# Kernel tuning notes

Measured on AMD Instinct MI355X. Metric: run time of the kernel, lower is better.

## Reference

```python
import jax, jax.numpy as jnp
import numpy as np

B, S, HIDDEN = 2, 2048, 2048
NUM_HEADS, NUM_KV_HEADS, HEAD_DIM = 16, 4, 128
Q_SIZE = NUM_HEADS * HEAD_DIM          # 2048
KV_SIZE = NUM_KV_HEADS * HEAD_DIM      # 512
ROPE_THETA = 10000.0
NEG = -1e30


def setup_inputs() -> dict:
    key = jax.random.key(0)
    k1, k2, k3 = jax.random.split(key, 3)
    hidden_states = jax.random.normal(k1, (B, S, HIDDEN), jnp.float32)
    w_qkv = jax.random.normal(k2, (HIDDEN, Q_SIZE + 2 * KV_SIZE), jnp.float32) / np.sqrt(HIDDEN)
    w_o = jax.random.normal(k3, (Q_SIZE, HIDDEN), jnp.float32) / np.sqrt(Q_SIZE)
    positions = jnp.broadcast_to(jnp.arange(S, dtype=jnp.int32), (B, S))
    return {"positions": positions, "hidden_states": hidden_states,
            "w_qkv": w_qkv, "w_o": w_o}


def _rope(x, positions):
    # x: [B, S, H, D], neox-style rotate-half rope over full head_dim
    d = x.shape[-1]
    inv_freq = 1.0 / (ROPE_THETA ** (jnp.arange(0, d, 2, dtype=jnp.float32) / d))
    ang = positions[..., None].astype(jnp.float32) * inv_freq      # [B, S, D/2]
    cos = jnp.cos(ang)[:, :, None, :]
    sin = jnp.sin(ang)[:, :, None, :]
    x1, x2 = jnp.split(x, 2, axis=-1)
    return jnp.concatenate([x1 * cos - x2 * sin, x2 * cos + x1 * sin], axis=-1)


def reference(positions, hidden_states, w_qkv, w_o):
    qkv = jnp.einsum('bsh,ho->bso', hidden_states, w_qkv)
    q, k, v = jnp.split(qkv, [Q_SIZE, Q_SIZE + KV_SIZE], axis=-1)
    q = q.reshape(B, S, NUM_HEADS, HEAD_DIM)
    k = k.reshape(B, S, NUM_KV_HEADS, HEAD_DIM)
    v = v.reshape(B, S, NUM_KV_HEADS, HEAD_DIM)
    q = _rope(q, positions)
    k = _rope(k, positions)
    rep = NUM_HEADS // NUM_KV_HEADS
    k = jnp.repeat(k, rep, axis=2)   # GQA expand -> [B, S, NUM_HEADS, D]
    v = jnp.repeat(v, rep, axis=2)
    scale = HEAD_DIM ** -0.5
    scores = jnp.einsum('bqhd,bkhd->bhqk', q, k) * scale   # [B, H, S, S]
    causal = jnp.tril(jnp.ones((S, S), dtype=bool))
    scores = jnp.where(causal, scores, NEG)
    probs = jax.nn.softmax(scores, axis=-1)
    attn = jnp.einsum('bhqk,bkhd->bqhd', probs, v).reshape(B, S, Q_SIZE)
    return jnp.einsum('bsq,qh->bsh', attn, w_o)
```

## Files before the change

### kernel.cpp

```cpp
#include <hip/hip_runtime.h>
#include <hip/hip_bf16.h>
#include <stdint.h>

#define BDIM 2
#define SDIM 2048
#define HID 2048
#define NH 16
#define NKV 4
#define HD 128
#define QSZ 2048
#define KVSZ 512
#define QKVW 3072
#define TOK (BDIM*SDIM)

typedef __attribute__((ext_vector_type(8))) short bf16x8;
typedef __attribute__((ext_vector_type(4))) float f32x4;
typedef __attribute__((ext_vector_type(16))) float f32x16;

__device__ __forceinline__ short f2bf(float f) {
  return (short)__bfloat16_as_ushort(__float2bfloat16(f));
}

__device__ __forceinline__ float exp2_fast(float x) {
  float r;
  asm("v_exp_f32 %0, %1" : "=v"(r) : "v"(x));
  return r;
}

__device__ __forceinline__ void sincos_rev(float rev, float* sn, float* cs) {
  float fr, s, c;
  asm("v_fract_f32 %0, %1" : "=v"(fr) : "v"(rev));
  asm("v_sin_f32 %0, %1" : "=v"(s) : "v"(fr));
  asm("v_cos_f32 %0, %1" : "=v"(c) : "v"(fr));
  *sn = s; *cs = c;
}

__device__ __forceinline__ int xcd_swz(int orig, int nwg) {
  int cpx = nwg >> 3;
  return (orig & 7) * cpx + (orig >> 3);
}

__device__ __forceinline__ void gload_lds16(const void* g, void* lds) {
  __builtin_amdgcn_global_load_lds(
      (const __attribute__((address_space(1))) void*)g,
      (__attribute__((address_space(3))) void*)lds, 16, 0, 0);
}

__global__ __launch_bounds__(256) void k_cvt_bf16(const float* __restrict__ in,
                                                  short* __restrict__ out, int n) {
  int i = (blockIdx.x * 256 + threadIdx.x) * 4;
  if (i >= n) return;
  float4 v = *(const float4*)(in + i);
  short4 o; o.x = f2bf(v.x); o.y = f2bf(v.y); o.z = f2bf(v.z); o.w = f2bf(v.w);
  *(short4*)(out + i) = o;
}

__global__ __launch_bounds__(256) void k_transpose_cvt(const float* __restrict__ in,
                                                       short* __restrict__ out,
                                                       int R, int C) {
  __shared__ short tile[64][65];
  int k0 = blockIdx.y * 64;
  int n0 = blockIdx.x * 64;
  int t = threadIdx.x;
#pragma unroll
  for (int i = 0; i < 16; ++i) {
    int idx = i * 256 + t;
    int kk = idx >> 6, nn = idx & 63;
    tile[kk][nn] = f2bf(in[(size_t)(k0 + kk) * C + n0 + nn]);
  }
  __syncthreads();
#pragma unroll
  for (int i = 0; i < 16; ++i) {
    int idx = i * 256 + t;
    int nn = idx >> 6, kk = idx & 63;
    out[(size_t)(n0 + nn) * R + k0 + kk] = tile[kk][nn];
  }
}

__global__ __launch_bounds__(256) void k_gemm_bf16(const short* __restrict__ A,
                                                   const short* __restrict__ Bt,
                                                   float* __restrict__ C,
                                                   int M, int N, int K) {
  __shared__ char lds[128 * 32 * 2 * 2];
  char* As = lds;
  char* Bs = lds + 8192;
  const int tid = threadIdx.x;
  const int w = tid >> 6, l = tid & 63;
  const int lq = l & 15, g = l >> 4;
  const int nx = N >> 7;
  const int bid = xcd_swz(blockIdx.x, nx * (M >> 7));
  const int m0 = (bid / nx) * 128, n0 = (bid % nx) * 128;
  const int wm = (w >> 1) * 64, wn = (w & 1) * 64;
  f32x4 acc[4][4] = {};

  const int nk = K >> 5;
  for (int kt = 0; kt < nk; ++kt) {
    const int k0 = kt * 32;
#pragma unroll
    for (int i = 0; i < 2; ++i) {
      int ch = (w + 4 * i) * 64 + l;
      int r = ch >> 2, cc = ch & 3;
      int gc = cc ^ ((r >> 1) & 3);
      gload_lds16(A + (size_t)(m0 + r) * K + k0 + gc * 8, As + (w + 4 * i) * 1024);
      gload_lds16(Bt + (size_t)(n0 + r) * K + k0 + gc * 8, Bs + (w + 4 * i) * 1024);
    }
    __syncthreads();
    bf16x8 af[4], bfr[4];
#pragma unroll
    for (int mi = 0; mi < 4; ++mi) {
      int row = wm + mi * 16 + lq;
      af[mi] = *(const bf16x8*)(As + row * 64 + ((g ^ ((row >> 1) & 3)) * 16));
    }
#pragma unroll
    for (int ni = 0; ni < 4; ++ni) {
      int row = wn + ni * 16 + lq;
      bfr[ni] = *(const bf16x8*)(Bs + row * 64 + ((g ^ ((row >> 1) & 3)) * 16));
    }
#pragma unroll
    for (int mi = 0; mi < 4; ++mi)
#pragma unroll
      for (int ni = 0; ni < 4; ++ni)
        acc[mi][ni] = __builtin_amdgcn_mfma_f32_16x16x32_bf16(af[mi], bfr[ni],
                                                              acc[mi][ni], 0, 0, 0);
    __syncthreads();
  }
#pragma unroll
  for (int mi = 0; mi < 4; ++mi)
#pragma unroll
    for (int ni = 0; ni < 4; ++ni)
#pragma unroll
      for (int r = 0; r < 4; ++r) {
        int row = m0 + wm + mi * 16 + 4 * g + r;
        int col = n0 + wn + ni * 16 + lq;
        C[(size_t)row * N + col] = acc[mi][ni][r];
      }
}

__global__ __launch_bounds__(256) void k_gemm_qkv_rope(const short* __restrict__ A,
                                                       const short* __restrict__ Bt,
                                                       const int* __restrict__ pos,
                                                       short* __restrict__ Qh,
                                                       short* __restrict__ Kh,
                                                       short* __restrict__ VT) {
  __shared__ char lds[128 * 32 * 2 * 2];
  char* As = lds;
  char* Bs = lds + 8192;
  const int tid = threadIdx.x;
  const int w = tid >> 6, l = tid & 63;
  const int lq = l & 15, g = l >> 4;
  const int bid = xcd_swz(blockIdx.x, (QKVW >> 7) * (TOK >> 7));
  const int hx = bid % (QKVW >> 7);
  const int m0 = (bid / (QKVW >> 7)) * 128, n0 = hx * 128;
  const int K = HID;
  f32x4 acc[2][8] = {};

  const int nk = K >> 5;
  for (int kt = 0; kt < nk; ++kt) {
    const int k0 = kt * 32;
#pragma unroll
    for (int i = 0; i < 2; ++i) {
      int ch = (w + 4 * i) * 64 + l;
      int r = ch >> 2, cc = ch & 3;
      int gc = cc ^ ((r >> 1) & 3);
      gload_lds16(A + (size_t)(m0 + r) * K + k0 + gc * 8, As + (w + 4 * i) * 1024);
      gload_lds16(Bt + (size_t)(n0 + r) * K + k0 + gc * 8, Bs + (w + 4 * i) * 1024);
    }
    __syncthreads();
    bf16x8 af[2], bfr[8];
#pragma unroll
    for (int mi = 0; mi < 2; ++mi) {
      int row = w * 32 + mi * 16 + lq;
      af[mi] = *(const bf16x8*)(As + row * 64 + ((g ^ ((row >> 1) & 3)) * 16));
    }
#pragma unroll
    for (int ni = 0; ni < 8; ++ni) {
      int row = ni * 16 + lq;
      bfr[ni] = *(const bf16x8*)(Bs + row * 64 + ((g ^ ((row >> 1) & 3)) * 16));
    }
#pragma unroll
    for (int mi = 0; mi < 2; ++mi)
#pragma unroll
      for (int ni = 0; ni < 8; ++ni)
        acc[mi][ni] = __builtin_amdgcn_mfma_f32_16x16x32_bf16(af[mi], bfr[ni],
                                                              acc[mi][ni], 0, 0, 0);
    __syncthreads();
  }

  const int b = m0 >> 11;
  if (hx < 20) {
    const float qscale = 0.12751743920f;
    const float sc = (hx < 16) ? qscale : 1.0f;
    short* dst = (hx < 16) ? (Qh + (size_t)(b * NH + hx) * SDIM * HD)
                           : (Kh + (size_t)(b * NKV + (hx - 16)) * SDIM * HD);
    float invf[4];
#pragma unroll
    for (int ni = 0; ni < 4; ++ni)
      invf[ni] = 0.15915494309f *
                 exp2_fast(-(float)(ni * 16 + lq) * (13.287712379549449f / 64.0f));
#pragma unroll
    for (int mi = 0; mi < 2; ++mi)
#pragma unroll
      for (int r = 0; r < 4; ++r) {
        int row = m0 + w * 32 + mi * 16 + 4 * g + r;
        int s = row & (SDIM - 1);
        float p = (float)pos[row];
        size_t hb = (size_t)s * HD;
#pragma unroll
        for (int ni = 0; ni < 4; ++ni) {
          float sn, cs;
          sincos_rev(p * invf[ni], &sn, &cs);
          float x1 = acc[mi][ni][r], x2 = acc[mi][ni + 4][r];
          dst[hb + ni * 16 + lq] = f2bf((x1 * cs - x2 * sn) * sc);
          dst[hb + ni * 16 + lq + 64] = f2bf((x2 * cs + x1 * sn) * sc);
        }
      }
  } else {
    const int hv = hx - 20;
    const int s00 = (m0 & (SDIM - 1)) + w * 32;
#pragma unroll
    for (int mi = 0; mi < 2; ++mi)
#pragma unroll
      for (int ni = 0; ni < 8; ++ni) {
        int d = ni * 16 + lq;
        int s0 = s00 + mi * 16 + 4 * g;
        size_t vb = ((size_t)(b * NKV + hv) * HD + d) * SDIM + s0;
        short4 ov;
        ov.x = f2bf(acc[mi][ni][0]); ov.y = f2bf(acc[mi][ni][1]);
        ov.z = f2bf(acc[mi][ni][2]); ov.w = f2bf(acc[mi][ni][3]);
        *(short4*)(VT + vb) = ov;
      }
  }
}

__global__ __launch_bounds__(256, 2) void k_attn(const short* __restrict__ Qh,
                                                 const short* __restrict__ Kh,
                                                 const short* __restrict__ VT,
                                                 short* __restrict__ attn, int S) {
  __shared__ char lds[2][32768];
  const int tid = threadIdx.x;
  const int w = tid >> 6, l = tid & 63;
  const int l31 = l & 31, hi = l >> 5;
  const int nqc = S / 128;
  const int bid = blockIdx.x;
  const int b = bid / (NH * nqc);
  const int rem = bid % (NH * nqc);
  const int h = rem / nqc;
  const int qc = nqc - 1 - (rem % nqc);
  const int q0 = qc * 128 + w * 32;
  const int kvh = h >> 2;
  const short* Qp = Qh + (size_t)(b * NH + h) * S * HD;
  const short* Kp = Kh + (size_t)(b * NKV + kvh) * S * HD;
  const short* Vp = VT + (size_t)(b * NKV + kvh) * HD * S;

  bf16x8 qf[8];
#pragma unroll
  for (int kc = 0; kc < 8; ++kc)
    qf[kc] = *(const bf16x8*)(Qp + (size_t)(q0 + l31) * HD + kc * 16 + hi * 8);

  f32x16 o[4] = {};
  float mrun = -1e30f, lrun = 0.f;
  const int qabs = q0 + l31;
  const int ntu = qc * 2 + 2;

#define STAGE(bufi, c0_)                                                          \
  {                                                                               \
    char* Kb = lds[bufi];                                                         \
    char* Vb = lds[bufi] + 16384;                                                 \
    _Pragma("unroll")                                                             \
    for (int i = 0; i < 4; ++i) {                                                 \
      int id = (i * 4 + w) * 64 + l;                                              \
      int kr = id >> 4, c16 = id & 15;                                            \
      gload_lds16(Kp + (size_t)((c0_) + kr) * HD + ((c16 ^ (kr & 15)) * 8),       \
                  Kb + (i * 4 + w) * 1024);                                       \
      int vr = id >> 3, c8 = id & 7;                                              \
      gload_lds16(Vp + (size_t)vr * S + (c0_) + ((c8 ^ (vr & 7)) * 8),            \
                  Vb + (i * 4 + w) * 1024);                                       \
    }                                                                             \
  }

  STAGE(0, 0);
  asm volatile("s_waitcnt vmcnt(0)" ::: "memory");
  __builtin_amdgcn_s_barrier();

  for (int c = 0; c < ntu; ++c) {
    const int c0 = c * 64;
    const int cur = c & 1;
    if (c + 1 < ntu) STAGE(cur ^ 1, c0 + 64);
    const char* Ks = lds[cur];
    const char* Vs = lds[cur] + 16384;

    f32x16 st[2];
    __builtin_amdgcn_s_setprio(1);
#pragma unroll
    for (int tt = 0; tt < 2; ++tt) {
      f32x16 s = {};
#pragma unroll
      for (int kc = 0; kc < 8; ++kc) {
        int kr = tt * 32 + l31;
        bf16x8 kf = *(const bf16x8*)(Ks + kr * 256 + (((kc * 2 + hi) ^ (l31 & 15)) * 16));
        s = __builtin_amdgcn_mfma_f32_32x32x16_bf16(kf, qf[kc], s, 0, 0, 0);
      }
      st[tt] = s;
    }
    __builtin_amdgcn_s_setprio(0);
    float tmax = -1e30f;
    if (c0 + 64 <= q0) {
#pragma unroll
      for (int tt = 0; tt < 2; ++tt)
#pragma unroll
        for (int r = 0; r < 16; ++r) tmax = fmaxf(tmax, st[tt][r]);
    } else {
#pragma unroll
      for (int tt = 0; tt < 2; ++tt)
#pragma unroll
        for (int r = 0; r < 16; ++r) {
          int kv = c0 + tt * 32 + (r & 3) + 8 * (r >> 2) + 4 * hi;
          float sv = (kv <= qabs) ? st[tt][r] : -1e30f;
          st[tt][r] = sv;
          tmax = fmaxf(tmax, sv);
        }
    }
    tmax = fmaxf(tmax, __shfl_xor(tmax, 32));
    if (!__all(tmax - mrun <= 8.0f)) {
      float mnew = fmaxf(mrun, tmax);
      float fac = exp2_fast(mrun - mnew);
      lrun *= fac;
#pragma unroll
      for (int d0 = 0; d0 < 4; ++d0) o[d0] = o[d0] * fac;
      mrun = mnew;
    }
    float sum = 0.f;
#pragma unroll
    for (int tt = 0; tt < 2; ++tt)
#pragma unroll
      for (int r = 0; r < 16; ++r) {
        float e = exp2_fast(st[tt][r] - mrun);
        st[tt][r] = e;
        sum += e;
      }
    sum += __shfl_xor(sum, 32);
    lrun += sum;
    __builtin_amdgcn_s_setprio(1);
#pragma unroll
    for (int j = 0; j < 4; ++j) {
      const int tt = j >> 1, kc = j & 1;
      uint32_t W0 = (uint32_t)(uint16_t)f2bf(st[tt][8 * kc + 0]) |
                    ((uint32_t)(uint16_t)f2bf(st[tt][8 * kc + 1]) << 16);
      uint32_t W1 = (uint32_t)(uint16_t)f2bf(st[tt][8 * kc + 2]) |
                    ((uint32_t)(uint16_t)f2bf(st[tt][8 * kc + 3]) << 16);
      uint32_t W2 = (uint32_t)(uint16_t)f2bf(st[tt][8 * kc + 4]) |
                    ((uint32_t)(uint16_t)f2bf(st[tt][8 * kc + 5]) << 16);
      uint32_t W3 = (uint32_t)(uint16_t)f2bf(st[tt][8 * kc + 6]) |
                    ((uint32_t)(uint16_t)f2bf(st[tt][8 * kc + 7]) << 16);
      uint32_t Y0 = __shfl_xor(hi ? W0 : W2, 32);
      uint32_t Y1 = __shfl_xor(hi ? W1 : W3, 32);
      union { uint32_t u[4]; bf16x8 v; } pu;
      pu.u[0] = hi ? Y0 : W0;
      pu.u[1] = hi ? Y1 : W1;
      pu.u[2] = hi ? W2 : Y0;
      pu.u[3] = hi ? W3 : Y1;
#pragma unroll
      for (int d0 = 0; d0 < 4; ++d0) {
        int vr = d0 * 32 + l31;
        bf16x8 vf = *(const bf16x8*)(Vs + vr * 128 + (((j * 2 + hi) ^ (vr & 7)) * 16));
        o[d0] = __builtin_amdgcn_mfma_f32_32x32x16_bf16(vf, pu.v, o[d0], 0, 0, 0);
      }
    }
    __builtin_amdgcn_s_setprio(0);
    asm volatile("s_waitcnt vmcnt(0)" ::: "memory");
    __builtin_amdgcn_s_barrier();
  }
#undef STAGE
  float inv = 1.0f / lrun;
  size_t rowb = (size_t)(b * S + q0 + l31) * QSZ + h * HD;
#pragma unroll
  for (int d0 = 0; d0 < 4; ++d0)
#pragma unroll
    for (int gq = 0; gq < 4; ++gq) {
      short4 ov;
      ov.x = f2bf(o[d0][4 * gq + 0] * inv);
      ov.y = f2bf(o[d0][4 * gq + 1] * inv);
      ov.z = f2bf(o[d0][4 * gq + 2] * inv);
      ov.w = f2bf(o[d0][4 * gq + 3] * inv);
      *(short4*)(attn + rowb + d0 * 32 + 8 * gq + 4 * hi) = ov;
    }
}

extern "C" void kernel_launch(void* const* d_in, const int* in_sizes, int n_in,
                              void* d_out, int out_size, void* d_ws, size_t ws_size,
                              hipStream_t stream) {
  const int* positions = (const int*)d_in[0];
  const float* hidden = (const float*)d_in[1];
  const float* w_qkv = (const float*)d_in[2];
  const float* w_o = (const float*)d_in[3];
  float* out = (float*)d_out;

  char* ws = (char*)d_ws;
  short* X     = (short*)(ws);
  short* WqkvT = (short*)(ws + 16777216);
  short* WoT   = (short*)(ws + 29360128);
  short* Qh    = (short*)(ws + 88080384);
  short* Kh    = (short*)(ws + 104857600);
  short* VT    = (short*)(ws + 109051904);
  short* ATT   = (short*)(ws + 113246208);

  k_cvt_bf16<<<8192, 256, 0, stream>>>(hidden, X, TOK * HID);
  k_transpose_cvt<<<dim3(QKVW / 64, HID / 64), 256, 0, stream>>>(w_qkv, WqkvT, HID, QKVW);
  k_transpose_cvt<<<dim3(HID / 64, QSZ / 64), 256, 0, stream>>>(w_o, WoT, QSZ, HID);
  k_gemm_qkv_rope<<<(QKVW / 128) * (TOK / 128), 256, 0, stream>>>(X, WqkvT, positions,
                                                                  Qh, Kh, VT);
  k_attn<<<BDIM * NH * (SDIM / 128), 256, 0, stream>>>(Qh, Kh, VT, ATT, SDIM);
  k_gemm_bf16<<<(HID / 128) * (TOK / 128), 256, 0, stream>>>(ATT, WoT, out, TOK, HID, QSZ);
}
```

Baseline: 221.5 us.

## Merge prep kernels into one launch and double GEMM K-tile to 64

Folds the hidden-state bf16 conversion and the two weight transpose-conversions into a single k_prep launch, dispatching on block index. Both GEMM kernels now stage a 64-wide K slice per iteration instead of 32, with an 8-way XOR swizzle for 128-byte LDS rows. This halves the barrier and loop overhead per unit of MFMA work and removes two kernel launches. In exchange LDS use doubles to 32 KB per block, which may reduce occupancy.

New measurement: 225.8 us. Within noise of the previous version (+1.9%).

```diff
diff --git a/kernel.cpp b/kernel.cpp
--- a/kernel.cpp
+++ b/kernel.cpp
@@ -46,22 +46,31 @@
       (__attribute__((address_space(3))) void*)lds, 16, 0, 0);
 }
 
-__global__ __launch_bounds__(256) void k_cvt_bf16(const float* __restrict__ in,
-                                                  short* __restrict__ out, int n) {
-  int i = (blockIdx.x * 256 + threadIdx.x) * 4;
-  if (i >= n) return;
-  float4 v = *(const float4*)(in + i);
-  short4 o; o.x = f2bf(v.x); o.y = f2bf(v.y); o.z = f2bf(v.z); o.w = f2bf(v.w);
-  *(short4*)(out + i) = o;
-}
-
-__global__ __launch_bounds__(256) void k_transpose_cvt(const float* __restrict__ in,
-                                                       short* __restrict__ out,
-                                                       int R, int C) {
+__global__ __launch_bounds__(256) void k_prep(const float* __restrict__ hidden,
+                                              const float* __restrict__ w_qkv,
+                                              const float* __restrict__ w_o,
+                                              short* __restrict__ X,
+                                              short* __restrict__ WqkvT,
+                                              short* __restrict__ WoT) {
   __shared__ short tile[64][65];
-  int k0 = blockIdx.y * 64;
-  int n0 = blockIdx.x * 64;
-  int t = threadIdx.x;
+  const int bid = blockIdx.x;
+  const int t = threadIdx.x;
+  if (bid < 8192) {
+    int i = (bid * 256 + t) * 4;
+    float4 v = *(const float4*)(hidden + i);
+    short4 o; o.x = f2bf(v.x); o.y = f2bf(v.y); o.z = f2bf(v.z); o.w = f2bf(v.w);
+    *(short4*)(X + i) = o;
+    return;
+  }
+  const float* in; short* out; int R, C, bx, by;
+  if (bid < 9728) {
+    int tt = bid - 8192; in = w_qkv; out = WqkvT; R = HID; C = QKVW;
+    bx = tt % 48; by = tt / 48;
+  } else {
+    int tt = bid - 9728; in = w_o; out = WoT; R = QSZ; C = HID;
+    bx = tt & 31; by = tt >> 5;
+  }
+  int k0 = by * 64, n0 = bx * 64;
 #pragma unroll
   for (int i = 0; i < 16; ++i) {
     int idx = i * 256 + t;
@@ -81,9 +90,9 @@
                                                    const short* __restrict__ Bt,
                                                    float* __restrict__ C,
                                                    int M, int N, int K) {
-  __shared__ char lds[128 * 32 * 2 * 2];
+  __shared__ char lds[32768];
   char* As = lds;
-  char* Bs = lds + 8192;
+  char* Bs = lds + 16384;
   const int tid = threadIdx.x;
   const int w = tid >> 6, l = tid & 63;
   const int lq = l & 15, g = l >> 4;
@@ -93,35 +102,38 @@
   const int wm = (w >> 1) * 64, wn = (w & 1) * 64;
   f32x4 acc[4][4] = {};
 
-  const int nk = K >> 5;
+  const int nk = K >> 6;
   for (int kt = 0; kt < nk; ++kt) {
-    const int k0 = kt * 32;
-#pragma unroll
-    for (int i = 0; i < 2; ++i) {
-      int ch = (w + 4 * i) * 64 + l;
-      int r = ch >> 2, cc = ch & 3;
-      int gc = cc ^ ((r >> 1) & 3);
-      gload_lds16(A + (size_t)(m0 + r) * K + k0 + gc * 8, As + (w + 4 * i) * 1024);
-      gload_lds16(Bt + (size_t)(n0 + r) * K + k0 + gc * 8, Bs + (w + 4 * i) * 1024);
+    const int k0 = kt * 64;
+#pragma unroll
+    for (int i = 0; i < 4; ++i) {
+      int ch = (i * 4 + w) * 64 + l;
+      int r = ch >> 3, cc = ch & 7;
+      int gc = cc ^ (r & 7);
+      gload_lds16(A + (size_t)(m0 + r) * K + k0 + gc * 8, As + (i * 4 + w) * 1024);
+      gload_lds16(Bt + (size_t)(n0 + r) * K + k0 + gc * 8, Bs + (i * 4 + w) * 1024);
     }
     __syncthreads();
-    bf16x8 af[4], bfr[4];
-#pragma unroll
-    for (int mi = 0; mi < 4; ++mi) {
-      int row = wm + mi * 16 + lq;
-      af[mi] = *(const bf16x8*)(As + row * 64 + ((g ^ ((row >> 1) & 3)) * 16));
-    }
-#pragma unroll
-    for (int ni = 0; ni < 4; ++ni) {
-      int row = wn + ni * 16 + lq;
-      bfr[ni] = *(const bf16x8*)(Bs + row * 64 + ((g ^ ((row >> 1) & 3)) * 16));
-    }
-#pragma unroll
-    for (int mi = 0; mi < 4; ++mi)
-#pragma unroll
-      for (int ni = 0; ni < 4; ++ni)
-        acc[mi][ni] = __builtin_amdgcn_mfma_f32_16x16x32_bf16(af[mi], bfr[ni],
-                                                              acc[mi][ni], 0, 0, 0);
+#pragma unroll
+    for (int kk = 0; kk < 2; ++kk) {
+      bf16x8 af[4], bfr[4];
+#pragma unroll
+      for (int mi = 0; mi < 4; ++mi) {
+        int row = wm + mi * 16 + lq;
+        af[mi] = *(const bf16x8*)(As + row * 128 + (((kk * 4 + g) ^ (row & 7)) * 16));
+      }
+#pragma unroll
+      for (int ni = 0; ni < 4; ++ni) {
+        int row = wn + ni * 16 + lq;
+        bfr[ni] = *(const bf16x8*)(Bs + row * 128 + (((kk * 4 + g) ^ (row & 7)) * 16));
+      }
+#pragma unroll
+      for (int mi = 0; mi < 4; ++mi)
+#pragma unroll
+        for (int ni = 0; ni < 4; ++ni)
+          acc[mi][ni] = __builtin_amdgcn_mfma_f32_16x16x32_bf16(af[mi], bfr[ni],
+                                                                acc[mi][ni], 0, 0, 0);
+    }
     __syncthreads();
   }
 #pragma unroll
@@ -142,9 +154,9 @@
                                                        short* __restrict__ Qh,
                                                        short* __restrict__ Kh,
                                                        short* __restrict__ VT) {
-  __shared__ char lds[128 * 32 * 2 * 2];
+  __shared__ char lds[32768];
   char* As = lds;
-  char* Bs = lds + 8192;
+  char* Bs = lds + 16384;
   const int tid = threadIdx.x;
   const int w = tid >> 6, l = tid & 63;
   const int lq = l & 15, g = l >> 4;
@@ -154,35 +166,38 @@
   const int K = HID;
   f32x4 acc[2][8] = {};
 
-  const int nk = K >> 5;
+  const int nk = K >> 6;
   for (int kt = 0; kt < nk; ++kt) {
-    const int k0 = kt * 32;
-#pragma unroll
-    for (int i = 0; i < 2; ++i) {
-      int ch = (w + 4 * i) * 64 + l;
-      int r = ch >> 2, cc = ch & 3;
-      int gc = cc ^ ((r >> 1) & 3);
-      gload_lds16(A + (size_t)(m0 + r) * K + k0 + gc * 8, As + (w + 4 * i) * 1024);
-      gload_lds16(Bt + (size_t)(n0 + r) * K + k0 + gc * 8, Bs + (w + 4 * i) * 1024);
+    const int k0 = kt * 64;
+#pragma unroll
+    for (int i = 0; i < 4; ++i) {
+      int ch = (i * 4 + w) * 64 + l;
+      int r = ch >> 3, cc = ch & 7;
+      int gc = cc ^ (r & 7);
+      gload_lds16(A + (size_t)(m0 + r) * K + k0 + gc * 8, As + (i * 4 + w) * 1024);
+      gload_lds16(Bt + (size_t)(n0 + r) * K + k0 + gc * 8, Bs + (i * 4 + w) * 1024);
     }
     __syncthreads();
-    bf16x8 af[2], bfr[8];
-#pragma unroll
-    for (int mi = 0; mi < 2; ++mi) {
-      int row = w * 32 + mi * 16 + lq;
-      af[mi] = *(const bf16x8*)(As + row * 64 + ((g ^ ((row >> 1) & 3)) * 16));
-    }
-#pragma unroll
-    for (int ni = 0; ni < 8; ++ni) {
-      int row = ni * 16 + lq;
-      bfr[ni] = *(const bf16x8*)(Bs + row * 64 + ((g ^ ((row >> 1) & 3)) * 16));
-    }
-#pragma unroll
-    for (int mi = 0; mi < 2; ++mi)
-#pragma unroll
-      for (int ni = 0; ni < 8; ++ni)
-        acc[mi][ni] = __builtin_amdgcn_mfma_f32_16x16x32_bf16(af[mi], bfr[ni],
-                                                              acc[mi][ni], 0, 0, 0);
+#pragma unroll
+    for (int kk = 0; kk < 2; ++kk) {
+      bf16x8 af[2], bfr[8];
+#pragma unroll
+      for (int mi = 0; mi < 2; ++mi) {
+        int row = w * 32 + mi * 16 + lq;
+        af[mi] = *(const bf16x8*)(As + row * 128 + (((kk * 4 + g) ^ (row & 7)) * 16));
+      }
+#pragma unroll
+      for (int ni = 0; ni < 8; ++ni) {
+        int row = ni * 16 + lq;
+        bfr[ni] = *(const bf16x8*)(Bs + row * 128 + (((kk * 4 + g) ^ (row & 7)) * 16));
+      }
+#pragma unroll
+      for (int mi = 0; mi < 2; ++mi)
+#pragma unroll
+        for (int ni = 0; ni < 8; ++ni)
+          acc[mi][ni] = __builtin_amdgcn_mfma_f32_16x16x32_bf16(af[mi], bfr[ni],
+                                                                acc[mi][ni], 0, 0, 0);
+    }
     __syncthreads();
   }
 
@@ -404,9 +419,7 @@
   short* VT    = (short*)(ws + 109051904);
   short* ATT   = (short*)(ws + 113246208);
 
-  k_cvt_bf16<<<8192, 256, 0, stream>>>(hidden, X, TOK * HID);
-  k_transpose_cvt<<<dim3(QKVW / 64, HID / 64), 256, 0, stream>>>(w_qkv, WqkvT, HID, QKVW);
-  k_transpose_cvt<<<dim3(HID / 64, QSZ / 64), 256, 0, stream>>>(w_o, WoT, QSZ, HID);
+  k_prep<<<10752, 256, 0, stream>>>(hidden, w_qkv, w_o, X, WqkvT, WoT);
   k_gemm_qkv_rope<<<(QKVW / 128) * (TOK / 128), 256, 0, stream>>>(X, WqkvT, positions,
                                                                   Qh, Kh, VT);
   k_attn<<<BDIM * NH * (SDIM / 128), 256, 0, stream>>>(Qh, Kh, VT, ATT, SDIM);
```
